# Performance work log

Hardware: AMD Instinct MI355X
Metric: run time of the kernel (lower is better)

The kernel has to match this reference:

```python
import jax, jax.numpy as jnp
import numpy as np

B, S, D, L = 32, 1024, 768, 12

def setup_inputs() -> dict:
    key = jax.random.key(0)
    ks = jax.random.split(key, 10)
    hidden_states = jax.random.normal(ks[0], (B, S, D), dtype=jnp.float32)
    Wq = jax.random.normal(ks[1], (L, D, D), dtype=jnp.float32) * 0.02
    Wk = jax.random.normal(ks[2], (L, D, D), dtype=jnp.float32) * 0.02
    Wv = jax.random.normal(ks[3], (L, D, D), dtype=jnp.float32) * 0.02
    bq = jnp.zeros((L, D), dtype=jnp.float32)
    bk = jnp.zeros((L, D), dtype=jnp.float32)
    bv = jnp.zeros((L, D), dtype=jnp.float32)
    l_k = jnp.full((L, D), 0.8, dtype=jnp.float32)  # iA3 scales, init 0.8 per source
    l_v = jnp.full((L, D), 0.8, dtype=jnp.float32)
    W_head = jax.random.normal(ks[4], (D, 1), dtype=jnp.float32) * 0.02
    b_head = jnp.zeros((1,), dtype=jnp.float32)
    return {"hidden_states": hidden_states, "Wq": Wq, "bq": bq, "Wk": Wk, "bk": bk,
            "Wv": Wv, "bv": bv, "l_k": l_k, "l_v": l_v, "W_head": W_head, "b_head": b_head}

def reference(hidden_states, Wq, bq, Wk, bk, Wv, bv, l_k, l_v, W_head, b_head):
    scale = 1.0 / jnp.sqrt(jnp.float32(D))

    def layer_step(h, params):
        wq, bq_i, wk, bk_i, wv, bv_i, lk, lv = params
        Q = jnp.einsum('bsd,de->bse', h, wq) + bq_i
        K = (jnp.einsum('bsd,de->bse', h, wk) + bk_i) * lk  # iA3 per-channel scale on K
        V = (jnp.einsum('bsd,de->bse', h, wv) + bv_i) * lv  # iA3 per-channel scale on V
        attn = jax.nn.softmax(jnp.einsum('bqd,bkd->bqk', Q, K) * scale, axis=-1)
        h_new = jnp.einsum('bqk,bkd->bqd', attn, V)  # note: no residual/LN, matches source
        return h_new, None

    h, _ = jax.lax.scan(layer_step, hidden_states, (Wq, bq, Wk, bk, Wv, bv, l_k, l_v))
    pooled = h[:, 0, :]  # CLS token
    out = pooled @ W_head + b_head  # [B, 1]
    return out[:, 0]
```

## Files before the change

kernel.cpp:

```cpp
#include <hip/hip_runtime.h>
#include <hip/hip_fp16.h>
#include <math.h>

#define B_ 32
#define S_ 1024
#define D_ 768
#define L_ 12
#define SD 786432LL
#define SS 1048576LL
#define DD 589824LL
#define LDL 1769472LL

typedef _Float16 half8 __attribute__((ext_vector_type(8)));
typedef float f32x4 __attribute__((ext_vector_type(4)));
typedef unsigned short u16;

#define SW(lr) ((((lr) ^ ((lr) >> 3)) & 7))

__global__ __launch_bounds__(256, 2)
void gemm_qkv_k(const __half* __restrict__ A, const __half* __restrict__ Wt,
                const float* __restrict__ biasC, const float* __restrict__ scaleC,
                float aBias,
                __half* __restrict__ CQ, __half* __restrict__ CK, __half* __restrict__ CVt,
                int nBase, int tilesX, int mPerXcd)
{
    __shared__ __align__(16) u16 smem[16384];
    const int K = 768;

    const int flat = blockIdx.x;
    const int xcd = flat & 7;
    const int jj = flat >> 3;
    const int mLocal = jj / tilesX;
    const int nxI = jj - mLocal * tilesX;
    const int n0 = nxI * 128;
    const int m0 = (xcd * mPerXcd + mLocal) * 128;

    const int t = threadIdx.x;
    const int l = t & 63, w = t >> 6;
    const int wm = (w & 1) * 64, wn = (w >> 1) * 64;

    const int u0 = t, u1 = t + 256;
    const int r0 = u0 >> 2, c0 = (u0 & 3) ^ (r0 & 3);
    const int r1 = u1 >> 2, c1 = (u1 & 3) ^ (r1 & 3);
    const __half* gA0 = A + (long long)(m0 + r0) * K + c0 * 8;
    const __half* gA1 = A + (long long)(m0 + r1) * K + c1 * 8;
    const __half* gB0 = Wt + (long long)(n0 + r0) * K + c0 * 8;
    const __half* gB1 = Wt + (long long)(n0 + r1) * K + c1 * 8;
    u16* lA0 = &smem[u0 * 8];
    u16* lA1 = &smem[u1 * 8];
    u16* lB0 = &smem[4096 + u0 * 8];
    u16* lB1 = &smem[4096 + u1 * 8];

    int aoff[4], boff[4];
    const int kc = l >> 4;
    #pragma unroll
    for (int mt = 0; mt < 4; ++mt) {
        int rr = wm + mt * 16 + (l & 15);
        aoff[mt] = (rr * 4 + (kc ^ (rr & 3))) * 8;
        int rb = wn + mt * 16 + (l & 15);
        boff[mt] = (rb * 4 + (kc ^ (rb & 3))) * 8;
    }

    f32x4 acc[4][4];
    #pragma unroll
    for (int i = 0; i < 4; ++i)
        #pragma unroll
        for (int j = 0; j < 4; ++j)
            acc[i][j] = (f32x4){0.f, 0.f, 0.f, 0.f};

    for (int k0 = 0; k0 < K; k0 += 32) {
        __builtin_amdgcn_global_load_lds((const __attribute__((address_space(1))) void*)(gA0 + k0),
                                         (__attribute__((address_space(3))) void*)lA0, 16, 0, 0);
        __builtin_amdgcn_global_load_lds((const __attribute__((address_space(1))) void*)(gA1 + k0),
                                         (__attribute__((address_space(3))) void*)lA1, 16, 0, 0);
        __builtin_amdgcn_global_load_lds((const __attribute__((address_space(1))) void*)(gB0 + k0),
                                         (__attribute__((address_space(3))) void*)lB0, 16, 0, 0);
        __builtin_amdgcn_global_load_lds((const __attribute__((address_space(1))) void*)(gB1 + k0),
                                         (__attribute__((address_space(3))) void*)lB1, 16, 0, 0);
        __syncthreads();

        half8 af[4], bf[4];
        #pragma unroll
        for (int mt = 0; mt < 4; ++mt) af[mt] = *(const half8*)(const void*)&smem[aoff[mt]];
        #pragma unroll
        for (int nt = 0; nt < 4; ++nt) bf[nt] = *(const half8*)(const void*)&smem[4096 + boff[nt]];

        #pragma unroll
        for (int nt = 0; nt < 4; ++nt)
            #pragma unroll
            for (int mt = 0; mt < 4; ++mt)
                acc[mt][nt] = __builtin_amdgcn_mfma_f32_16x16x32_f16(af[mt], bf[nt], acc[mt][nt], 0, 0, 0);
        __syncthreads();
    }

    const int nCat0 = n0 + nBase;
    const int region = nCat0 / 768;
    const int colBase = nCat0 - region * 768;

    float badd[4], bmul[4];
    #pragma unroll
    for (int nt = 0; nt < 4; ++nt) {
        int gn = nCat0 + wn + nt * 16 + (l & 15);
        badd[nt] = aBias * biasC[gn];
        bmul[nt] = scaleC[gn];
    }

    const int qbase = w * 4096;
    #pragma unroll
    for (int mt = 0; mt < 4; ++mt) {
        #pragma unroll
        for (int nt = 0; nt < 4; ++nt) {
            #pragma unroll
            for (int i = 0; i < 4; ++i) {
                int lrow = mt * 16 + ((l >> 4) << 2) + i;
                int lcol = nt * 16 + (l & 15);
                float v = (acc[mt][nt][i] + badd[nt]) * bmul[nt];
                int cc = lcol >> 3, c7 = lcol & 7;
                smem[qbase + lrow * 64 + ((cc ^ SW(lrow)) << 3) + c7] =
                    __half_as_ushort(__float2half(v));
            }
        }
    }
    __syncthreads();

    if (region < 2) {
        __half* Creg = region ? CK : CQ;
        #pragma unroll
        for (int p = 0; p < 8; ++p) {
            int u = t + p * 256;
            int R = u >> 4, cc = u & 15;
            int qb = ((R >> 6) + ((cc >> 3) << 1)) * 4096;
            int lr = R & 63, lcc = cc & 7;
            half8 val = *(const half8*)(const void*)&smem[qb + lr * 64 + ((lcc ^ SW(lr)) << 3)];
            *(half8*)(void*)&Creg[(long long)(m0 + R) * 768 + colBase + cc * 8] = val;
        }
    } else {
        #pragma unroll
        for (int p = 0; p < 8; ++p) {
            int u = t + p * 256;
            int Crow = u >> 4, mcc = u & 15;
            __align__(16) u16 tmp[8];
            #pragma unroll
            for (int j = 0; j < 8; ++j) {
                int m = mcc * 8 + j;
                int qb = ((m >> 6) + ((Crow >> 6) << 1)) * 4096;
                int lr = m & 63, lcol = Crow & 63;
                int lcc = lcol >> 3;
                tmp[j] = smem[qb + lr * 64 + ((lcc ^ SW(lr)) << 3) + (lcol & 7)];
            }
            long long b = m0 >> 10;
            __half* dst = CVt + b * SD + (long long)(colBase + Crow) * 1024 + (m0 & 1023) + mcc * 8;
            *(half8*)(void*)dst = *(const half8*)(const void*)tmp;
        }
    }
}

template<int SWIZ, int MODE>
__global__ __launch_bounds__(256, 2)
void gemm_att_k(const __half* __restrict__ A, const __half* __restrict__ B,
                float aAcc, __half* __restrict__ C, int K, int ldc,
                long long sA, long long sB, long long sC,
                int tilesX, int tilesPB, int bpx,
                float* __restrict__ rsp, const float* __restrict__ invsum)
{
    __shared__ __align__(16) u16 smem[16384];
    __shared__ float sums[128 * 17];

    int nxI, ny;
    long long bz;
    if (SWIZ) {
        int flat = blockIdx.x;
        int xcd = flat & 7;
        int j = flat >> 3;
        int bLocal = j / tilesPB;
        int tt = j - bLocal * tilesPB;
        bz = (long long)(xcd * bpx + bLocal);
        ny = tt / tilesX;
        nxI = tt - ny * tilesX;
    } else {
        nxI = blockIdx.x; ny = blockIdx.y; bz = blockIdx.z;
    }

    const int t = threadIdx.x;
    const int l = t & 63, w = t >> 6;
    const int n0 = nxI * 128;
    const int m0 = ny * 128;
    A += bz * sA; B += bz * sB; C += bz * sC;

    const int wm = (w & 1) * 64, wn = (w >> 1) * 64;

    const int u0 = t, u1 = t + 256;
    const int r0 = u0 >> 2, c0 = (u0 & 3) ^ (r0 & 3);
    const int r1 = u1 >> 2, c1 = (u1 & 3) ^ (r1 & 3);
    const __half* gA0 = A + (long long)(m0 + r0) * K + c0 * 8;
    const __half* gA1 = A + (long long)(m0 + r1) * K + c1 * 8;
    const __half* gB0 = B + (long long)(n0 + r0) * K + c0 * 8;
    const __half* gB1 = B + (long long)(n0 + r1) * K + c1 * 8;
    u16* lA0 = &smem[u0 * 8];
    u16* lA1 = &smem[u1 * 8];
    u16* lB0 = &smem[4096 + u0 * 8];
    u16* lB1 = &smem[4096 + u1 * 8];

    int aoff[4], boff[4];
    const int kc = l >> 4;
    #pragma unroll
    for (int mt = 0; mt < 4; ++mt) {
        int rr = wm + mt * 16 + (l & 15);
        aoff[mt] = (rr * 4 + (kc ^ (rr & 3))) * 8;
        int rb = wn + mt * 16 + (l & 15);
        boff[mt] = (rb * 4 + (kc ^ (rb & 3))) * 8;
    }

    f32x4 acc[4][4];
    #pragma unroll
    for (int i = 0; i < 4; ++i)
        #pragma unroll
        for (int j = 0; j < 4; ++j)
            acc[i][j] = (f32x4){0.f, 0.f, 0.f, 0.f};

    for (int k0 = 0; k0 < K; k0 += 32) {
        __builtin_amdgcn_global_load_lds((const __attribute__((address_space(1))) void*)(gA0 + k0),
                                         (__attribute__((address_space(3))) void*)lA0, 16, 0, 0);
        __builtin_amdgcn_global_load_lds((const __attribute__((address_space(1))) void*)(gA1 + k0),
                                         (__attribute__((address_space(3))) void*)lA1, 16, 0, 0);
        __builtin_amdgcn_global_load_lds((const __attribute__((address_space(1))) void*)(gB0 + k0),
                                         (__attribute__((address_space(3))) void*)lB0, 16, 0, 0);
        __builtin_amdgcn_global_load_lds((const __attribute__((address_space(1))) void*)(gB1 + k0),
                                         (__attribute__((address_space(3))) void*)lB1, 16, 0, 0);
        __syncthreads();

        half8 af[4], bf[4];
        #pragma unroll
        for (int mt = 0; mt < 4; ++mt) af[mt] = *(const half8*)(const void*)&smem[aoff[mt]];
        #pragma unroll
        for (int nt = 0; nt < 4; ++nt) bf[nt] = *(const half8*)(const void*)&smem[4096 + boff[nt]];

        #pragma unroll
        for (int nt = 0; nt < 4; ++nt)
            #pragma unroll
            for (int mt = 0; mt < 4; ++mt)
                acc[mt][nt] = __builtin_amdgcn_mfma_f32_16x16x32_f16(af[mt], bf[nt], acc[mt][nt], 0, 0, 0);
        __syncthreads();
    }

    float invr[4][4];
    if (MODE == 2) {
        #pragma unroll
        for (int mt = 0; mt < 4; ++mt)
            #pragma unroll
            for (int i = 0; i < 4; ++i)
                invr[mt][i] = invsum[bz * 1024 + m0 + wm + mt * 16 + ((l >> 4) << 2) + i];
    }

    const int qbase = w * 4096;
    #pragma unroll
    for (int mt = 0; mt < 4; ++mt) {
        #pragma unroll
        for (int nt = 0; nt < 4; ++nt) {
            #pragma unroll
            for (int i = 0; i < 4; ++i) {
                int lrow = mt * 16 + ((l >> 4) << 2) + i;
                int lcol = nt * 16 + (l & 15);
                float v;
                if (MODE == 1)      v = __expf(acc[mt][nt][i] * aAcc);
                else                v = acc[mt][nt][i] * aAcc * invr[mt][i];
                int cc = lcol >> 3, c7 = lcol & 7;
                smem[qbase + lrow * 64 + ((cc ^ SW(lrow)) << 3) + c7] =
                    __half_as_ushort(__float2half(v));
            }
        }
    }
    __syncthreads();

    #pragma unroll
    for (int p = 0; p < 8; ++p) {
        int u = t + p * 256;
        int R = u >> 4, cc = u & 15;
        int qb = ((R >> 6) + ((cc >> 3) << 1)) * 4096;
        int lr = R & 63, lcc = cc & 7;
        half8 val = *(const half8*)(const void*)&smem[qb + lr * 64 + ((lcc ^ SW(lr)) << 3)];
        *(half8*)(void*)&C[(long long)(m0 + R) * ldc + n0 + cc * 8] = val;
        if (MODE == 1) {
            float s8 = 0.f;
            #pragma unroll
            for (int j = 0; j < 8; ++j) s8 += (float)val[j];
            sums[R * 17 + cc] = s8;
        }
    }
    if (MODE == 1) {
        __syncthreads();
        if (t < 128) {
            float s = 0.f;
            #pragma unroll
            for (int c = 0; c < 16; ++c) s += sums[t * 17 + c];
            rsp[bz * 8192 + (long long)(m0 + t) * 8 + nxI] = s;
        }
    }
}

__global__ __launch_bounds__(256)
void rowsuminv_k(const float* __restrict__ rsp, float* __restrict__ inv, int n)
{
    int i = blockIdx.x * 256 + threadIdx.x;
    if (i < n) {
        const float* p = rsp + (long long)i * 8;
        float s = ((p[0] + p[1]) + (p[2] + p[3])) + ((p[4] + p[5]) + (p[6] + p[7]));
        inv[i] = 1.0f / s;
    }
}

__global__ __launch_bounds__(256)
void cvt32to16_k(const float* __restrict__ X, __half* __restrict__ Y)
{
    long long i = ((long long)blockIdx.x * 256 + threadIdx.x) * 4;
    float4 v = *(const float4*)&X[i];
    *(__half2*)&Y[i]     = __floats2half2_rn(v.x, v.y);
    *(__half2*)&Y[i + 2] = __floats2half2_rn(v.z, v.w);
}

__global__ __launch_bounds__(256)
void wtrans_k(const float* __restrict__ W, __half* __restrict__ Wt,
              long long ldL, int rowOff)
{
    __shared__ float Ls[64][65];
    const int lyr = blockIdx.z;
    const int k0 = blockIdx.y * 64, n0 = blockIdx.x * 64;
    const float* src = W + (long long)lyr * DD;
    __half* dst = Wt + (long long)lyr * ldL;
    const int t = threadIdx.x;
    #pragma unroll
    for (int p = 0; p < 4; ++p) {
        int u = t + p * 256;
        int r = u >> 4, c4 = (u & 15) * 4;
        float4 v = *(const float4*)&src[(long long)(k0 + r) * D_ + n0 + c4];
        Ls[r][c4] = v.x; Ls[r][c4 + 1] = v.y; Ls[r][c4 + 2] = v.z; Ls[r][c4 + 3] = v.w;
    }
    __syncthreads();
    #pragma unroll
    for (int p = 0; p < 2; ++p) {
        int u = t + p * 256;
        int n = u >> 3, kc8 = (u & 7) * 8;
        __align__(16) u16 tmp[8];
        #pragma unroll
        for (int j = 0; j < 8; ++j) {
            _Float16 h = (_Float16)Ls[kc8 + j][n];
            tmp[j] = *(const u16*)&h;
        }
        *(half8*)(void*)&dst[(long long)(rowOff + n0 + n) * D_ + k0 + kc8] =
            *(const half8*)(const void*)tmp;
    }
}

__global__ __launch_bounds__(256)
void bscat_k(const float* __restrict__ bq, const float* __restrict__ bk,
             const float* __restrict__ bv, const float* __restrict__ lk,
             const float* __restrict__ lv, float* __restrict__ bsb,
             float* __restrict__ bss)
{
    int i = blockIdx.x * 256 + threadIdx.x;
    if (i >= L_ * 2304) return;
    int l = i / 2304, p = i - l * 2304;
    int r = p / 768, c = p - r * 768;
    float b, s;
    if (r == 0)      { b = bq[l * 768 + c]; s = 1.f; }
    else if (r == 1) { b = bk[l * 768 + c]; s = lk[l * 768 + c]; }
    else             { b = bv[l * 768 + c]; s = lv[l * 768 + c]; }
    bsb[i] = b; bss[i] = s;
}

__global__ __launch_bounds__(256)
void q0_k(const __half* __restrict__ H16, const __half* __restrict__ Wcat,
          const float* __restrict__ bq, float* __restrict__ q0f, float sig)
{
    const int b = blockIdx.x;
    const int n = blockIdx.y * 256 + threadIdx.x;
    const int t = threadIdx.x;
    __shared__ __half hrow[768];
    const __half* h = H16 + (long long)b * SD;
    hrow[t] = h[t]; hrow[t + 256] = h[t + 256]; hrow[t + 512] = h[t + 512];
    __syncthreads();
    const __half* wr = Wcat + 11LL * LDL + (long long)n * 768;
    float acc = 0.f;
    for (int k = 0; k < 768; ++k) acc += (float)hrow[k] * (float)wr[k];
    q0f[b * 768 + n] = acc + sig * bq[11 * 768 + n];
}

__global__ __launch_bounds__(256)
void s0_k(const float* __restrict__ q0f, const __half* __restrict__ K16,
          float* __restrict__ s0f, int b0, float aQK)
{
    const int z = blockIdx.x;
    const int b = b0 + z;
    const int s = blockIdx.y * 256 + threadIdx.x;
    const int t = threadIdx.x;
    __shared__ float qrow[768];
    qrow[t] = q0f[b * 768 + t];
    qrow[t + 256] = q0f[b * 768 + t + 256];
    qrow[t + 512] = q0f[b * 768 + t + 512];
    __syncthreads();
    const __half* kr = K16 + (long long)z * SD + (long long)s * 768;
    float acc = 0.f;
    for (int k = 0; k < 768; ++k) acc += qrow[k] * (float)kr[k];
    s0f[b * 1024 + s] = acc * aQK;
}

__global__ __launch_bounds__(256)
void sm0_k(float* __restrict__ s0f, int b0)
{
    float* p = s0f + (long long)(b0 + blockIdx.x) * 1024;
    const int t = threadIdx.x;
    float v[4];
    float mx = -1e30f;
    #pragma unroll
    for (int j = 0; j < 4; ++j) { v[j] = p[t + 256 * j]; mx = fmaxf(mx, v[j]); }
    __shared__ float red[256];
    red[t] = mx; __syncthreads();
    for (int s = 128; s > 0; s >>= 1) { if (t < s) red[t] = fmaxf(red[t], red[t + s]); __syncthreads(); }
    mx = red[0];
    __syncthreads();
    float sum = 0.f;
    #pragma unroll
    for (int j = 0; j < 4; ++j) { v[j] = __expf(v[j] - mx); sum += v[j]; }
    red[t] = sum; __syncthreads();
    for (int s = 128; s > 0; s >>= 1) { if (t < s) red[t] += red[t + s]; __syncthreads(); }
    const float inv = 1.0f / red[0];
    __syncthreads();
    #pragma unroll
    for (int j = 0; j < 4; ++j) p[t + 256 * j] = v[j] * inv;
}

__global__ __launch_bounds__(256)
void o0_k(const float* __restrict__ p0f, const __half* __restrict__ Vt16,
          float* __restrict__ o0f, int b0, float invSig)
{
    const int z = blockIdx.x;
    const int b = b0 + z;
    const int d = blockIdx.y * 256 + threadIdx.x;
    const int t = threadIdx.x;
    __shared__ float prow[1024];
    #pragma unroll
    for (int j = 0; j < 4; ++j) prow[t + 256 * j] = p0f[b * 1024 + t + 256 * j];
    __syncthreads();
    const __half* vr = Vt16 + (long long)z * SD + (long long)d * 1024;
    float acc = 0.f;
    for (int s = 0; s < 1024; ++s) acc += prow[s] * (float)vr[s];
    o0f[b * 768 + d] = acc * invSig;
}

__global__ __launch_bounds__(256)
void headf_k(const float* __restrict__ o0f, const float* __restrict__ Wh,
             const float* __restrict__ bh, float* __restrict__ out)
{
    const int b = blockIdx.x;
    const int t = threadIdx.x;
    float s = 0.f;
    for (int d = t; d < 768; d += 256) s += o0f[b * 768 + d] * Wh[d];
    __shared__ float red[256];
    red[t] = s; __syncthreads();
    for (int k = 128; k > 0; k >>= 1) { if (t < k) red[t] += red[t + k]; __syncthreads(); }
    if (t == 0) out[b] = red[0] + bh[0];
}

extern "C" void kernel_launch(void* const* d_in, const int* in_sizes, int n_in,
                              void* d_out, int out_size, void* d_ws, size_t ws_size,
                              hipStream_t stream)
{
    const float* hs = (const float*)d_in[0];
    const float* Wq = (const float*)d_in[1];
    const float* bq = (const float*)d_in[2];
    const float* Wk = (const float*)d_in[3];
    const float* bk = (const float*)d_in[4];
    const float* Wv = (const float*)d_in[5];
    const float* bv = (const float*)d_in[6];
    const float* lk = (const float*)d_in[7];
    const float* lv = (const float*)d_in[8];
    const float* Wh = (const float*)d_in[9];
    const float* bh = (const float*)d_in[10];
    float* outp = (float*)d_out;

    __half* H16  = (__half*)d_ws;
    __half* Wcat = H16 + (long long)B_ * SD;
    float*  bsb  = (float*)(Wcat + 12LL * LDL);
    float*  bss  = bsb + 12 * 2304;
    float*  q0f  = bss + 12 * 2304;
    float*  s0f  = q0f + 32 * 768;
    float*  o0f  = s0f + 32 * 1024;
    float*  rsp  = o0f + 32 * 768;
    float*  inv  = rsp + 32LL * 8192;
    __half* Q16  = (__half*)(inv + 32 * 1024);

    const size_t baseBytes = (size_t)((char*)Q16 - (char*)d_ws);
    const size_t perG = ((size_t)(3 * SD) + (size_t)SS) * 2;
    long long avail = (long long)ws_size - (long long)baseBytes;
    int G = (avail > 0) ? (int)(avail / perG) : 1;
    if (G >= 32) G = 32; else if (G >= 16) G = 16; else if (G >= 8) G = 8;
    if (G < 1) G = 1;
    __half* K16  = Q16 + (long long)G * SD;
    __half* Vt16 = K16 + (long long)G * SD;
    __half* P16  = Vt16 + (long long)G * SD;

    cvt32to16_k<<<dim3((int)((B_ * SD) / 1024)), 256, 0, stream>>>(hs, H16);
    wtrans_k<<<dim3(12, 12, 12), 256, 0, stream>>>(Wq, Wcat, LDL, 0);
    wtrans_k<<<dim3(12, 12, 12), 256, 0, stream>>>(Wk, Wcat, LDL, 768);
    wtrans_k<<<dim3(12, 12, 12), 256, 0, stream>>>(Wv, Wcat, LDL, 1536);
    bscat_k<<<dim3((L_ * 2304 + 255) / 256), 256, 0, stream>>>(bq, bk, bv, lk, lv, bsb, bss);

    const float scq = 0.036084391824351615f;
    float sig = 1.f;

    for (int lyr = 0; lyr < L_ - 1; ++lyr) {
        const __half* W = Wcat + (long long)lyr * LDL;
        const float* bb = bsb + lyr * 2304;
        const float* ss = bss + lyr * 2304;
        const float aQK = scq / (sig * sig);

        for (int b0 = 0; b0 < B_; b0 += G) {
            const int nb = (B_ - b0 < G) ? (B_ - b0) : G;
            const __half* hg = H16 + (long long)b0 * SD;

            gemm_qkv_k<<<dim3(18 * 8 * nb), 256, 0, stream>>>(
                hg, W, bb, ss, sig, Q16, K16, Vt16, 0, 18, nb);

            if ((nb & 7) == 0) {
                gemm_att_k<1, 1><<<dim3(nb * 64), 256, 0, stream>>>(
                    Q16, K16, aQK, P16, 768, 1024, SD, SD, SS, 8, 64, nb >> 3, rsp, nullptr);
            } else {
                gemm_att_k<0, 1><<<dim3(8, 8, nb), 256, 0, stream>>>(
                    Q16, K16, aQK, P16, 768, 1024, SD, SD, SS, 8, 64, 1, rsp, nullptr);
            }

            rowsuminv_k<<<dim3(nb * 4), 256, 0, stream>>>(rsp, inv, nb * 1024);

            if ((nb & 7) == 0) {
                gemm_att_k<1, 2><<<dim3(nb * 48), 256, 0, stream>>>(
                    P16, Vt16, 4.f, H16 + (long long)b0 * SD, 1024, 768, SS, SD, SD,
                    6, 48, nb >> 3, nullptr, inv);
            } else {
                gemm_att_k<0, 2><<<dim3(6, 8, nb), 256, 0, stream>>>(
                    P16, Vt16, 4.f, H16 + (long long)b0 * SD, 1024, 768, SS, SD, SD,
                    6, 48, 1, nullptr, inv);
            }
        }
        sig *= 4.f;
    }

    const float aQK = scq / (sig * sig);
    q0_k<<<dim3(B_, 3), 256, 0, stream>>>(H16, Wcat, bq, q0f, sig);

    for (int b0 = 0; b0 < B_; b0 += G) {
        const int nb = (B_ - b0 < G) ? (B_ - b0) : G;
        const __half* hg = H16 + (long long)b0 * SD;

        gemm_qkv_k<<<dim3(12 * 8 * nb), 256, 0, stream>>>(
            hg, Wcat + 11LL * LDL + 768LL * 768, bsb + 11 * 2304, bss + 11 * 2304,
            sig, K16 , K16, Vt16, 768, 12, nb);

        s0_k<<<dim3(nb, 4), 256, 0, stream>>>(q0f, K16, s0f, b0, aQK);
        sm0_k<<<dim3(nb), 256, 0, stream>>>(s0f, b0);
        o0_k<<<dim3(nb, 3), 256, 0, stream>>>(s0f, Vt16, o0f, b0, 1.f / sig);
    }

    headf_k<<<dim3(B_), 256, 0, stream>>>(o0f, Wh, bh, outp);
}
```

Before: 3.553 ms.

## Rewrite QKV GEMM with 256x256 tiles and a 4-stage async LDS pipeline

```diff
diff --git a/kernel.cpp b/kernel.cpp
--- a/kernel.cpp
+++ b/kernel.cpp
@@ -17,81 +17,123 @@
 
 #define SW(lr) ((((lr) ^ ((lr) >> 3)) & 7))
 
-__global__ __launch_bounds__(256, 2)
-void gemm_qkv_k(const __half* __restrict__ A, const __half* __restrict__ Wt,
-                const float* __restrict__ biasC, const float* __restrict__ scaleC,
-                float aBias,
-                __half* __restrict__ CQ, __half* __restrict__ CK, __half* __restrict__ CVt,
-                int nBase, int tilesX, int mPerXcd)
-{
-    __shared__ __align__(16) u16 smem[16384];
+template<int SWIZ>
+__global__ __launch_bounds__(512, 2)
+void gemm_qkv2_k(const __half* __restrict__ A, const __half* __restrict__ Wt,
+                 const float* __restrict__ biasC, const float* __restrict__ scaleC,
+                 float aBias,
+                 __half* __restrict__ CQ, __half* __restrict__ CK, __half* __restrict__ CVt,
+                 int nBase, int tilesX, int mPerXcd)
+{
+    __shared__ __align__(16) u16 smem[65536];
     const int K = 768;
 
-    const int flat = blockIdx.x;
-    const int xcd = flat & 7;
-    const int jj = flat >> 3;
-    const int mLocal = jj / tilesX;
-    const int nxI = jj - mLocal * tilesX;
-    const int n0 = nxI * 128;
-    const int m0 = (xcd * mPerXcd + mLocal) * 128;
+    int mIdx, nxI;
+    if (SWIZ) {
+        const int flat = blockIdx.x;
+        const int xcd = flat & 7;
+        const int jj = flat >> 3;
+        const int mLocal = jj / tilesX;
+        nxI = jj - mLocal * tilesX;
+        mIdx = xcd * mPerXcd + mLocal;
+    } else {
+        mIdx = blockIdx.x / tilesX;
+        nxI = blockIdx.x - mIdx * tilesX;
+    }
+    const int m0 = mIdx * 256;
+    const int n0 = nxI * 256;
 
     const int t = threadIdx.x;
     const int l = t & 63, w = t >> 6;
-    const int wm = (w & 1) * 64, wn = (w >> 1) * 64;
-
-    const int u0 = t, u1 = t + 256;
-    const int r0 = u0 >> 2, c0 = (u0 & 3) ^ (r0 & 3);
-    const int r1 = u1 >> 2, c1 = (u1 & 3) ^ (r1 & 3);
-    const __half* gA0 = A + (long long)(m0 + r0) * K + c0 * 8;
-    const __half* gA1 = A + (long long)(m0 + r1) * K + c1 * 8;
-    const __half* gB0 = Wt + (long long)(n0 + r0) * K + c0 * 8;
-    const __half* gB1 = Wt + (long long)(n0 + r1) * K + c1 * 8;
-    u16* lA0 = &smem[u0 * 8];
-    u16* lA1 = &smem[u1 * 8];
-    u16* lB0 = &smem[4096 + u0 * 8];
-    u16* lB1 = &smem[4096 + u1 * 8];
-
-    int aoff[4], boff[4];
-    const int kc = l >> 4;
-    #pragma unroll
-    for (int mt = 0; mt < 4; ++mt) {
-        int rr = wm + mt * 16 + (l & 15);
-        aoff[mt] = (rr * 4 + (kc ^ (rr & 3))) * 8;
-        int rb = wn + mt * 16 + (l & 15);
-        boff[mt] = (rb * 4 + (kc ^ (rb & 3))) * 8;
-    }
-
-    f32x4 acc[4][4];
-    #pragma unroll
-    for (int i = 0; i < 4; ++i)
+    const int wr = w & 1, wc = w >> 1;
+    const int q = l >> 4, lr = l & 15;
+
+    const int pA0 = t, pA1 = t + 512;
+    const int rA0 = pA0 >> 2, rA1 = pA1 >> 2;
+    const int kA0 = (pA0 & 3) ^ ((rA0 >> 1) & 3);
+    const int kA1 = (pA1 & 3) ^ ((rA1 >> 1) & 3);
+    const __half* gA0 = A + (long long)(m0 + rA0) * K + kA0 * 8;
+    const __half* gA1 = A + (long long)(m0 + rA1) * K + kA1 * 8;
+    const __half* gB0 = Wt + (long long)(n0 + rA0) * K + kA0 * 8;
+    const __half* gB1 = Wt + (long long)(n0 + rA1) * K + kA1 * 8;
+
+    int aoff[2][4], boff[4];
+    #pragma unroll
+    for (int mh = 0; mh < 2; ++mh)
+        #pragma unroll
+        for (int mt = 0; mt < 4; ++mt) {
+            int r = wr * 128 + mh * 64 + mt * 16 + lr;
+            aoff[mh][mt] = (r * 4 + (q ^ ((r >> 1) & 3))) * 8;
+        }
+    #pragma unroll
+    for (int nt = 0; nt < 4; ++nt) {
+        int r = wc * 64 + nt * 16 + lr;
+        boff[nt] = (r * 4 + (q ^ ((r >> 1) & 3))) * 8;
+    }
+
+    f32x4 acc[8][4];
+    #pragma unroll
+    for (int i = 0; i < 8; ++i)
         #pragma unroll
         for (int j = 0; j < 4; ++j)
             acc[i][j] = (f32x4){0.f, 0.f, 0.f, 0.f};
 
-    for (int k0 = 0; k0 < K; k0 += 32) {
-        __builtin_amdgcn_global_load_lds((const __attribute__((address_space(1))) void*)(gA0 + k0),
-                                         (__attribute__((address_space(3))) void*)lA0, 16, 0, 0);
-        __builtin_amdgcn_global_load_lds((const __attribute__((address_space(1))) void*)(gA1 + k0),
-                                         (__attribute__((address_space(3))) void*)lA1, 16, 0, 0);
-        __builtin_amdgcn_global_load_lds((const __attribute__((address_space(1))) void*)(gB0 + k0),
-                                         (__attribute__((address_space(3))) void*)lB0, 16, 0, 0);
-        __builtin_amdgcn_global_load_lds((const __attribute__((address_space(1))) void*)(gB1 + k0),
-                                         (__attribute__((address_space(3))) void*)lB1, 16, 0, 0);
-        __syncthreads();
-
-        half8 af[4], bf[4];
-        #pragma unroll
-        for (int mt = 0; mt < 4; ++mt) af[mt] = *(const half8*)(const void*)&smem[aoff[mt]];
-        #pragma unroll
-        for (int nt = 0; nt < 4; ++nt) bf[nt] = *(const half8*)(const void*)&smem[4096 + boff[nt]];
-
-        #pragma unroll
-        for (int nt = 0; nt < 4; ++nt)
+#define GLD(srcp, dstoff) \
+    __builtin_amdgcn_global_load_lds((const __attribute__((address_space(1))) void*)(srcp), \
+        (__attribute__((address_space(3))) void*)&smem[dstoff], 16, 0, 0)
+#define STAGE_A(d2, s2) do { GLD(gA0 + (s2) * 32, (d2) * 8192 + pA0 * 8); \
+                             GLD(gA1 + (s2) * 32, (d2) * 8192 + pA1 * 8); } while (0)
+#define STAGE_B(d2, s2) do { GLD(gB0 + (s2) * 32, 32768 + (d2) * 8192 + pA0 * 8); \
+                             GLD(gB1 + (s2) * 32, 32768 + (d2) * 8192 + pA1 * 8); } while (0)
+
+    STAGE_A(0, 0); STAGE_B(0, 0);
+    STAGE_A(1, 1); STAGE_B(1, 1);
+
+    for (int sB = 0; sB < 24; sB += 4) {
+        #pragma unroll
+        for (int j = 0; j < 4; ++j) {
+            const int s = sB + j;
+            if (s < 23) asm volatile("s_waitcnt vmcnt(4)\n\ts_barrier" ::: "memory");
+            else        asm volatile("s_waitcnt vmcnt(0)\n\ts_barrier" ::: "memory");
+
+            const int sa = j * 8192, sb = 32768 + j * 8192;
+            const int d2 = (j + 2) & 3;
+
+            if (s + 2 < 24) STAGE_A(d2, s + 2);
+            half8 bf[4], af[4];
+            #pragma unroll
+            for (int nt = 0; nt < 4; ++nt)
+                bf[nt] = *(const half8*)(const void*)&smem[sb + boff[nt]];
             #pragma unroll
             for (int mt = 0; mt < 4; ++mt)
-                acc[mt][nt] = __builtin_amdgcn_mfma_f32_16x16x32_f16(af[mt], bf[nt], acc[mt][nt], 0, 0, 0);
-        __syncthreads();
-    }
+                af[mt] = *(const half8*)(const void*)&smem[sa + aoff[0][mt]];
+            __builtin_amdgcn_s_setprio(1);
+            #pragma unroll
+            for (int nt = 0; nt < 4; ++nt)
+                #pragma unroll
+                for (int mt = 0; mt < 4; ++mt)
+                    acc[mt][nt] = __builtin_amdgcn_mfma_f32_16x16x32_f16(af[mt], bf[nt], acc[mt][nt], 0, 0, 0);
+            __builtin_amdgcn_s_setprio(0);
+
+            if (s + 2 < 24) STAGE_B(d2, s + 2);
+            half8 af2[4];
+            #pragma unroll
+            for (int mt = 0; mt < 4; ++mt)
+                af2[mt] = *(const half8*)(const void*)&smem[sa + aoff[1][mt]];
+            __builtin_amdgcn_s_setprio(1);
+            #pragma unroll
+            for (int nt = 0; nt < 4; ++nt)
+                #pragma unroll
+                for (int mt = 0; mt < 4; ++mt)
+                    acc[4 + mt][nt] = __builtin_amdgcn_mfma_f32_16x16x32_f16(af2[mt], bf[nt], acc[4 + mt][nt], 0, 0, 0);
+            __builtin_amdgcn_s_setprio(0);
+        }
+    }
+#undef STAGE_A
+#undef STAGE_B
+#undef GLD
+
+    __syncthreads();
 
     const int nCat0 = n0 + nBase;
     const int region = nCat0 / 768;
@@ -100,56 +142,52 @@
     float badd[4], bmul[4];
     #pragma unroll
     for (int nt = 0; nt < 4; ++nt) {
-        int gn = nCat0 + wn + nt * 16 + (l & 15);
+        int gn = nCat0 + wc * 64 + nt * 16 + lr;
         badd[nt] = aBias * biasC[gn];
         bmul[nt] = scaleC[gn];
     }
 
-    const int qbase = w * 4096;
-    #pragma unroll
-    for (int mt = 0; mt < 4; ++mt) {
-        #pragma unroll
-        for (int nt = 0; nt < 4; ++nt) {
-            #pragma unroll
-            for (int i = 0; i < 4; ++i) {
-                int lrow = mt * 16 + ((l >> 4) << 2) + i;
-                int lcol = nt * 16 + (l & 15);
-                float v = (acc[mt][nt][i] + badd[nt]) * bmul[nt];
-                int cc = lcol >> 3, c7 = lcol & 7;
-                smem[qbase + lrow * 64 + ((cc ^ SW(lrow)) << 3) + c7] =
-                    __half_as_ushort(__float2half(v));
-            }
-        }
-    }
+    #pragma unroll
+    for (int mh = 0; mh < 2; ++mh)
+        #pragma unroll
+        for (int mt = 0; mt < 4; ++mt)
+            #pragma unroll
+            for (int nt = 0; nt < 4; ++nt)
+                #pragma unroll
+                for (int i = 0; i < 4; ++i) {
+                    int lrow = wr * 128 + mh * 64 + mt * 16 + q * 4 + i;
+                    int lcol = wc * 64 + nt * 16 + lr;
+                    float v = (acc[mh * 4 + mt][nt][i] + badd[nt]) * bmul[nt];
+                    int kk = (lrow & 7) ^ ((lrow >> 3) & 7);
+                    smem[lrow * 256 + (((lcol >> 3) ^ kk) << 3) + (lcol & 7)] =
+                        __half_as_ushort(__float2half(v));
+                }
     __syncthreads();
 
     if (region < 2) {
         __half* Creg = region ? CK : CQ;
         #pragma unroll
-        for (int p = 0; p < 8; ++p) {
-            int u = t + p * 256;
-            int R = u >> 4, cc = u & 15;
-            int qb = ((R >> 6) + ((cc >> 3) << 1)) * 4096;
-            int lr = R & 63, lcc = cc & 7;
-            half8 val = *(const half8*)(const void*)&smem[qb + lr * 64 + ((lcc ^ SW(lr)) << 3)];
-            *(half8*)(void*)&Creg[(long long)(m0 + R) * 768 + colBase + cc * 8] = val;
+        for (int p = 0; p < 16; ++p) {
+            int u = t + p * 512;
+            int row = u >> 5, c = u & 31;
+            int kk = (row & 7) ^ ((row >> 3) & 7);
+            half8 val = *(const half8*)(const void*)&smem[row * 256 + ((c ^ kk) << 3)];
+            *(half8*)(void*)&Creg[(long long)(m0 + row) * 768 + colBase + c * 8] = val;
         }
     } else {
-        #pragma unroll
-        for (int p = 0; p < 8; ++p) {
-            int u = t + p * 256;
-            int Crow = u >> 4, mcc = u & 15;
+        long long b = m0 >> 10;
+        #pragma unroll
+        for (int p = 0; p < 16; ++p) {
+            int u = t + p * 512;
+            int ncol = u >> 5, m8 = u & 31;
             __align__(16) u16 tmp[8];
             #pragma unroll
-            for (int j = 0; j < 8; ++j) {
-                int m = mcc * 8 + j;
-                int qb = ((m >> 6) + ((Crow >> 6) << 1)) * 4096;
-                int lr = m & 63, lcol = Crow & 63;
-                int lcc = lcol >> 3;
-                tmp[j] = smem[qb + lr * 64 + ((lcc ^ SW(lr)) << 3) + (lcol & 7)];
+            for (int jj2 = 0; jj2 < 8; ++jj2) {
+                int row = m8 * 8 + jj2;
+                int kk = (row & 7) ^ ((row >> 3) & 7);
+                tmp[jj2] = smem[row * 256 + ((((ncol >> 3) ^ kk)) << 3) + (ncol & 7)];
             }
-            long long b = m0 >> 10;
-            __half* dst = CVt + b * SD + (long long)(colBase + Crow) * 1024 + (m0 & 1023) + mcc * 8;
+            __half* dst = CVt + b * SD + (long long)(colBase + ncol) * 1024 + (m0 & 1023) + m8 * 8;
             *(half8*)(void*)dst = *(const half8*)(const void*)tmp;
         }
     }
@@ -518,8 +556,13 @@
             const int nb = (B_ - b0 < G) ? (B_ - b0) : G;
             const __half* hg = H16 + (long long)b0 * SD;
 
-            gemm_qkv_k<<<dim3(18 * 8 * nb), 256, 0, stream>>>(
-                hg, W, bb, ss, sig, Q16, K16, Vt16, 0, 18, nb);
+            if ((nb & 1) == 0) {
+                gemm_qkv2_k<1><<<dim3(36 * nb), 512, 0, stream>>>(
+                    hg, W, bb, ss, sig, Q16, K16, Vt16, 0, 9, nb >> 1);
+            } else {
+                gemm_qkv2_k<0><<<dim3(36 * nb), 512, 0, stream>>>(
+                    hg, W, bb, ss, sig, Q16, K16, Vt16, 0, 9, 0);
+            }
 
             if ((nb & 7) == 0) {
                 gemm_att_k<1, 1><<<dim3(nb * 64), 256, 0, stream>>>(
@@ -551,9 +594,15 @@
         const int nb = (B_ - b0 < G) ? (B_ - b0) : G;
         const __half* hg = H16 + (long long)b0 * SD;
 
-        gemm_qkv_k<<<dim3(12 * 8 * nb), 256, 0, stream>>>(
-            hg, Wcat + 11LL * LDL + 768LL * 768, bsb + 11 * 2304, bss + 11 * 2304,
-            sig, K16 , K16, Vt16, 768, 12, nb);
+        if ((nb & 1) == 0) {
+            gemm_qkv2_k<1><<<dim3(24 * nb), 512, 0, stream>>>(
+                hg, Wcat + 11LL * LDL + 768LL * 768, bsb + 11 * 2304, bss + 11 * 2304,
+                sig, K16 , K16, Vt16, 768, 6, nb >> 1);
+        } else {
+            gemm_qkv2_k<0><<<dim3(24 * nb), 512, 0, stream>>>(
+                hg, Wcat + 11LL * LDL + 768LL * 768, bsb + 11 * 2304, bss + 11 * 2304,
+                sig, K16 , K16, Vt16, 768, 6, 0);
+        }
 
         s0_k<<<dim3(nb, 4), 256, 0, stream>>>(q0f, K16, s0f, b0, aQK);
         sm0_k<<<dim3(nb), 256, 0, stream>>>(s0f, b0);
```

Result: slower. 3.828 ms (+7.8%).

## Double-buffer LDS tiles and prefetch next K-slice during MFMA in GEMM kernels

Applied to the files above, without the earlier changes.

```diff
diff --git a/kernel.cpp b/kernel.cpp
--- a/kernel.cpp
+++ b/kernel.cpp
@@ -17,6 +17,10 @@
 
 #define SW(lr) ((((lr) ^ ((lr) >> 3)) & 7))
 
+#define GLD16(p, o) __builtin_amdgcn_global_load_lds( \
+        (const __attribute__((address_space(1))) void*)(p), \
+        (__attribute__((address_space(3))) void*)&smem[o], 16, 0, 0)
+
 __global__ __launch_bounds__(256, 2)
 void gemm_qkv_k(const __half* __restrict__ A, const __half* __restrict__ Wt,
                 const float* __restrict__ biasC, const float* __restrict__ scaleC,
@@ -40,25 +44,21 @@
     const int wm = (w & 1) * 64, wn = (w >> 1) * 64;
 
     const int u0 = t, u1 = t + 256;
-    const int r0 = u0 >> 2, c0 = (u0 & 3) ^ (r0 & 3);
-    const int r1 = u1 >> 2, c1 = (u1 & 3) ^ (r1 & 3);
+    const int r0 = u0 >> 2, c0 = (u0 & 3) ^ ((r0 >> 1) & 3);
+    const int r1 = u1 >> 2, c1 = (u1 & 3) ^ ((r1 >> 1) & 3);
     const __half* gA0 = A + (long long)(m0 + r0) * K + c0 * 8;
     const __half* gA1 = A + (long long)(m0 + r1) * K + c1 * 8;
     const __half* gB0 = Wt + (long long)(n0 + r0) * K + c0 * 8;
     const __half* gB1 = Wt + (long long)(n0 + r1) * K + c1 * 8;
-    u16* lA0 = &smem[u0 * 8];
-    u16* lA1 = &smem[u1 * 8];
-    u16* lB0 = &smem[4096 + u0 * 8];
-    u16* lB1 = &smem[4096 + u1 * 8];
 
     int aoff[4], boff[4];
     const int kc = l >> 4;
     #pragma unroll
     for (int mt = 0; mt < 4; ++mt) {
         int rr = wm + mt * 16 + (l & 15);
-        aoff[mt] = (rr * 4 + (kc ^ (rr & 3))) * 8;
+        aoff[mt] = (rr * 4 + (kc ^ ((rr >> 1) & 3))) * 8;
         int rb = wn + mt * 16 + (l & 15);
-        boff[mt] = (rb * 4 + (kc ^ (rb & 3))) * 8;
+        boff[mt] = (rb * 4 + (kc ^ ((rb >> 1) & 3))) * 8;
     }
 
     f32x4 acc[4][4];
@@ -68,29 +68,31 @@
         for (int j = 0; j < 4; ++j)
             acc[i][j] = (f32x4){0.f, 0.f, 0.f, 0.f};
 
+    GLD16(gA0, u0 * 8);         GLD16(gA1, u1 * 8);
+    GLD16(gB0, 8192 + u0 * 8);  GLD16(gB1, 8192 + u1 * 8);
+    asm volatile("s_waitcnt vmcnt(0)\n\ts_barrier" ::: "memory");
+
+    int cur = 0;
     for (int k0 = 0; k0 < K; k0 += 32) {
-        __builtin_amdgcn_global_load_lds((const __attribute__((address_space(1))) void*)(gA0 + k0),
-                                         (__attribute__((address_space(3))) void*)lA0, 16, 0, 0);
-        __builtin_amdgcn_global_load_lds((const __attribute__((address_space(1))) void*)(gA1 + k0),
-                                         (__attribute__((address_space(3))) void*)lA1, 16, 0, 0);
-        __builtin_amdgcn_global_load_lds((const __attribute__((address_space(1))) void*)(gB0 + k0),
-                                         (__attribute__((address_space(3))) void*)lB0, 16, 0, 0);
-        __builtin_amdgcn_global_load_lds((const __attribute__((address_space(1))) void*)(gB1 + k0),
-                                         (__attribute__((address_space(3))) void*)lB1, 16, 0, 0);
-        __syncthreads();
-
+        const int sa = cur * 4096, sb = 8192 + cur * 4096;
         half8 af[4], bf[4];
         #pragma unroll
-        for (int mt = 0; mt < 4; ++mt) af[mt] = *(const half8*)(const void*)&smem[aoff[mt]];
-        #pragma unroll
-        for (int nt = 0; nt < 4; ++nt) bf[nt] = *(const half8*)(const void*)&smem[4096 + boff[nt]];
-
+        for (int mt = 0; mt < 4; ++mt) af[mt] = *(const half8*)(const void*)&smem[sa + aoff[mt]];
+        #pragma unroll
+        for (int nt = 0; nt < 4; ++nt) bf[nt] = *(const half8*)(const void*)&smem[sb + boff[nt]];
+        __builtin_amdgcn_sched_barrier(0);
+        if (k0 + 32 < K) {
+            const int nsa = (cur ^ 1) * 4096, nsb = 8192 + (cur ^ 1) * 4096;
+            GLD16(gA0 + k0 + 32, nsa + u0 * 8);  GLD16(gA1 + k0 + 32, nsa + u1 * 8);
+            GLD16(gB0 + k0 + 32, nsb + u0 * 8);  GLD16(gB1 + k0 + 32, nsb + u1 * 8);
+        }
         #pragma unroll
         for (int nt = 0; nt < 4; ++nt)
             #pragma unroll
             for (int mt = 0; mt < 4; ++mt)
                 acc[mt][nt] = __builtin_amdgcn_mfma_f32_16x16x32_f16(af[mt], bf[nt], acc[mt][nt], 0, 0, 0);
-        __syncthreads();
+        asm volatile("s_waitcnt vmcnt(0)\n\ts_barrier" ::: "memory");
+        cur ^= 1;
     }
 
     const int nCat0 = n0 + nBase;
@@ -190,25 +192,21 @@
     const int wm = (w & 1) * 64, wn = (w >> 1) * 64;
 
     const int u0 = t, u1 = t + 256;
-    const int r0 = u0 >> 2, c0 = (u0 & 3) ^ (r0 & 3);
-    const int r1 = u1 >> 2, c1 = (u1 & 3) ^ (r1 & 3);
+    const int r0 = u0 >> 2, c0 = (u0 & 3) ^ ((r0 >> 1) & 3);
+    const int r1 = u1 >> 2, c1 = (u1 & 3) ^ ((r1 >> 1) & 3);
     const __half* gA0 = A + (long long)(m0 + r0) * K + c0 * 8;
     const __half* gA1 = A + (long long)(m0 + r1) * K + c1 * 8;
     const __half* gB0 = B + (long long)(n0 + r0) * K + c0 * 8;
     const __half* gB1 = B + (long long)(n0 + r1) * K + c1 * 8;
-    u16* lA0 = &smem[u0 * 8];
-    u16* lA1 = &smem[u1 * 8];
-    u16* lB0 = &smem[4096 + u0 * 8];
-    u16* lB1 = &smem[4096 + u1 * 8];
 
     int aoff[4], boff[4];
     const int kc = l >> 4;
     #pragma unroll
     for (int mt = 0; mt < 4; ++mt) {
         int rr = wm + mt * 16 + (l & 15);
-        aoff[mt] = (rr * 4 + (kc ^ (rr & 3))) * 8;
+        aoff[mt] = (rr * 4 + (kc ^ ((rr >> 1) & 3))) * 8;
         int rb = wn + mt * 16 + (l & 15);
-        boff[mt] = (rb * 4 + (kc ^ (rb & 3))) * 8;
+        boff[mt] = (rb * 4 + (kc ^ ((rb >> 1) & 3))) * 8;
     }
 
     f32x4 acc[4][4];
@@ -218,29 +216,31 @@
         for (int j = 0; j < 4; ++j)
             acc[i][j] = (f32x4){0.f, 0.f, 0.f, 0.f};
 
+    GLD16(gA0, u0 * 8);         GLD16(gA1, u1 * 8);
+    GLD16(gB0, 8192 + u0 * 8);  GLD16(gB1, 8192 + u1 * 8);
+    asm volatile("s_waitcnt vmcnt(0)\n\ts_barrier" ::: "memory");
+
+    int cur = 0;
     for (int k0 = 0; k0 < K; k0 += 32) {
-        __builtin_amdgcn_global_load_lds((const __attribute__((address_space(1))) void*)(gA0 + k0),
-                                         (__attribute__((address_space(3))) void*)lA0, 16, 0, 0);
-        __builtin_amdgcn_global_load_lds((const __attribute__((address_space(1))) void*)(gA1 + k0),
-                                         (__attribute__((address_space(3))) void*)lA1, 16, 0, 0);
-        __builtin_amdgcn_global_load_lds((const __attribute__((address_space(1))) void*)(gB0 + k0),
-                                         (__attribute__((address_space(3))) void*)lB0, 16, 0, 0);
-        __builtin_amdgcn_global_load_lds((const __attribute__((address_space(1))) void*)(gB1 + k0),
-                                         (__attribute__((address_space(3))) void*)lB1, 16, 0, 0);
-        __syncthreads();
-
+        const int sa = cur * 4096, sb = 8192 + cur * 4096;
         half8 af[4], bf[4];
         #pragma unroll
-        for (int mt = 0; mt < 4; ++mt) af[mt] = *(const half8*)(const void*)&smem[aoff[mt]];
-        #pragma unroll
-        for (int nt = 0; nt < 4; ++nt) bf[nt] = *(const half8*)(const void*)&smem[4096 + boff[nt]];
-
+        for (int mt = 0; mt < 4; ++mt) af[mt] = *(const half8*)(const void*)&smem[sa + aoff[mt]];
+        #pragma unroll
+        for (int nt = 0; nt < 4; ++nt) bf[nt] = *(const half8*)(const void*)&smem[sb + boff[nt]];
+        __builtin_amdgcn_sched_barrier(0);
+        if (k0 + 32 < K) {
+            const int nsa = (cur ^ 1) * 4096, nsb = 8192 + (cur ^ 1) * 4096;
+            GLD16(gA0 + k0 + 32, nsa + u0 * 8);  GLD16(gA1 + k0 + 32, nsa + u1 * 8);
+            GLD16(gB0 + k0 + 32, nsb + u0 * 8);  GLD16(gB1 + k0 + 32, nsb + u1 * 8);
+        }
         #pragma unroll
         for (int nt = 0; nt < 4; ++nt)
             #pragma unroll
             for (int mt = 0; mt < 4; ++mt)
                 acc[mt][nt] = __builtin_amdgcn_mfma_f32_16x16x32_f16(af[mt], bf[nt], acc[mt][nt], 0, 0, 0);
-        __syncthreads();
+        asm volatile("s_waitcnt vmcnt(0)\n\ts_barrier" ::: "memory");
+        cur ^= 1;
     }
 
     float invr[4][4];
```

After: 3.623 ms. Within noise of the previous version (+2.0%).
